# Optimization experiments

Measured on AMD Instinct MI355X. Metric: run time of the kernel, lower is better.

Reference implementation:

```python
import jax, jax.numpy as jnp
import numpy as np

NUM_EXPERTS = 8
TOP_K = 2
AUX_COEF = 0.01
B, S, D, H = 4, 2048, 1024, 684


def setup_inputs() -> dict:
    key = jax.random.key(0)
    ks = jax.random.split(key, 5)
    scale_d = 1.0 / np.sqrt(D)
    scale_h = 1.0 / np.sqrt(H)
    return {
        "x": jax.random.normal(ks[0], (B, S, D), dtype=jnp.float32),
        "router_w": jax.random.normal(ks[1], (NUM_EXPERTS, D), dtype=jnp.float32) * scale_d,
        "w1": jax.random.normal(ks[2], (NUM_EXPERTS, H, D), dtype=jnp.float32) * scale_d,
        "w2": jax.random.normal(ks[3], (NUM_EXPERTS, D, H), dtype=jnp.float32) * scale_h,
        "w3": jax.random.normal(ks[4], (NUM_EXPERTS, H, D), dtype=jnp.float32) * scale_d,
    }


def reference(x, router_w, w1, w2, w3):
    b, s, d = x.shape
    xf = x.reshape(-1, d)                                   # [T, d]
    probs = jax.nn.softmax(xf @ router_w.T, axis=-1)        # [T, E]
    topk_probs, topk_idx = jax.lax.top_k(probs, TOP_K)      # [T, k]

    # aux load-balancing loss (uses top-1 assignment density)
    density = jnp.mean(jax.nn.one_hot(topk_idx[:, 0], NUM_EXPERTS, dtype=xf.dtype), axis=0)
    aux_loss = AUX_COEF * jnp.sum(density * probs.mean(axis=0)) * NUM_EXPERTS

    # per-token per-expert combine weight (sums probs if an expert repeats across slots)
    combine = jnp.sum(jax.nn.one_hot(topk_idx, NUM_EXPERTS, dtype=xf.dtype)
                      * topk_probs[..., None], axis=1)      # [T, E]

    out = jnp.zeros_like(xf)
    for e in range(NUM_EXPERTS):  # fixed small expert loop
        h = jax.nn.silu(xf @ w1[e].T) * (xf @ w3[e].T)      # [T, H] SwiGLU
        out = out + combine[:, e:e + 1] * (h @ w2[e].T)     # weighted scatter-combine
    return out.reshape(b, s, d), aux_loss
```

## Files before the change

### kernel.cpp

```cpp
#include <hip/hip_runtime.h>
#include <hip/hip_bf16.h>

#define T_TOK 8192
#define DMODEL 1024
#define HDIM 684
#define HPAD 704
#define NEXP 8

typedef short  bf16x8  __attribute__((ext_vector_type(8)));
typedef float  f32x4   __attribute__((ext_vector_type(4)));

__device__ inline unsigned short f2bu(float f) {
    __hip_bfloat16 h = __float2bfloat16(f);
    return *reinterpret_cast<unsigned short*>(&h);
}

typedef const __attribute__((address_space(1))) unsigned int* gas_p;
typedef __attribute__((address_space(3))) unsigned int* las_p;
__device__ inline void ld_lds16(const unsigned short* g, unsigned short* l) {
    __builtin_amdgcn_global_load_lds((gas_p)g, (las_p)l, 16, 0, 0);
}

#define POS_OFF    74252800ull
#define PAIRS_OFF  74318336ull
#define WS_NEED   141427200ull

__global__ __launch_bounds__(256) void cvt_all(
    const float* __restrict__ w1, const float* __restrict__ w3, const float* __restrict__ w2,
    unsigned short* __restrict__ w1b, unsigned short* __restrict__ w3b,
    unsigned short* __restrict__ w2b, int n4, int n2)
{
    int i = blockIdx.x * 256 + threadIdx.x;
    if (i < 2 * n4) {
        const float* src; unsigned short* dst; int j;
        if (i < n4) { src = w1; dst = w1b; j = i; }
        else        { src = w3; dst = w3b; j = i - n4; }
        float4 v = ((const float4*)src)[j];
        ((ushort4*)dst)[j] = make_ushort4(f2bu(v.x), f2bu(v.y), f2bu(v.z), f2bu(v.w));
        return;
    }
    int j = i - 2 * n4;
    if (j >= n2) return;
    int row = j / 176;
    int col = (j - row * 176) * 4;
    ushort4 o = make_ushort4(0, 0, 0, 0);
    if (col < HDIM) {
        float4 v = *(const float4*)(w2 + (size_t)row * HDIM + col);
        o = make_ushort4(f2bu(v.x), f2bu(v.y), f2bu(v.z), f2bu(v.w));
    }
    *(ushort4*)(w2b + (size_t)row * HPAD + col) = o;
}

__global__ __launch_bounds__(256) void moe_router(
    const float* __restrict__ x, const float* __restrict__ rw,
    unsigned short* __restrict__ xb,
    float* __restrict__ blk_psum, int* __restrict__ blk_t1, int* __restrict__ blk_pc,
    int* __restrict__ topk_idx, float* __restrict__ topk_p)
{
    __shared__ float sp[4][NEXP];
    __shared__ int   si1[4], si2[4];

    int lane = threadIdx.x & 63;
    int w    = threadIdx.x >> 6;
    int t    = blockIdx.x * 4 + w;
    const float4* xr4 = (const float4*)(x + (size_t)t * DMODEL);
    ushort4* xbr4 = (ushort4*)(xb + (size_t)t * DMODEL);

    float acc[NEXP];
#pragma unroll
    for (int e = 0; e < NEXP; ++e) acc[e] = 0.f;
#pragma unroll
    for (int j = 0; j < DMODEL / 256; ++j) {
        float4 xv = xr4[j * 64 + lane];
        xbr4[j * 64 + lane] = make_ushort4(f2bu(xv.x), f2bu(xv.y), f2bu(xv.z), f2bu(xv.w));
#pragma unroll
        for (int e = 0; e < NEXP; ++e) {
            float4 rv = ((const float4*)(rw + (size_t)e * DMODEL))[j * 64 + lane];
            acc[e] += xv.x * rv.x + xv.y * rv.y + xv.z * rv.z + xv.w * rv.w;
        }
    }
#pragma unroll
    for (int off = 32; off > 0; off >>= 1) {
#pragma unroll
        for (int e = 0; e < NEXP; ++e)
            acc[e] += __shfl_xor(acc[e], off, 64);
    }
    if (lane == 0) {
        float m = acc[0];
#pragma unroll
        for (int e = 1; e < NEXP; ++e) m = fmaxf(m, acc[e]);
        float p[NEXP]; float s = 0.f;
#pragma unroll
        for (int e = 0; e < NEXP; ++e) { p[e] = expf(acc[e] - m); s += p[e]; }
        float inv = 1.f / s;
#pragma unroll
        for (int e = 0; e < NEXP; ++e) p[e] *= inv;
        int i1 = 0;
#pragma unroll
        for (int e = 1; e < NEXP; ++e) if (p[e] > p[i1]) i1 = e;
        int i2 = (i1 == 0) ? 1 : 0;
#pragma unroll
        for (int e = 0; e < NEXP; ++e) if (e != i1 && p[e] > p[i2]) i2 = e;

        topk_idx[t * 2 + 0] = i1;  topk_idx[t * 2 + 1] = i2;
        topk_p[t * 2 + 0] = p[i1]; topk_p[t * 2 + 1] = p[i2];
#pragma unroll
        for (int e = 0; e < NEXP; ++e) sp[w][e] = p[e];
        si1[w] = i1; si2[w] = i2;
    }
    __syncthreads();
    if (threadIdx.x < NEXP) {
        int e = threadIdx.x;
        float ps = sp[0][e] + sp[1][e] + sp[2][e] + sp[3][e];
        int t1 = (si1[0] == e) + (si1[1] == e) + (si1[2] == e) + (si1[3] == e);
        int pc = t1 + (si2[0] == e) + (si2[1] == e) + (si2[2] == e) + (si2[3] == e);
        blk_psum[blockIdx.x * NEXP + e] = ps;
        blk_t1[blockIdx.x * NEXP + e]  = t1;
        blk_pc[blockIdx.x * NEXP + e]  = pc;
    }
}

__global__ __launch_bounds__(256) void moe_scan(
    const float* __restrict__ blk_psum, const int* __restrict__ blk_t1,
    const int* __restrict__ blk_pc,
    int* pair_count, int* offsets, int* cursor, float* aux_out)
{
    __shared__ float wp[4][NEXP];
    __shared__ int   wt[4][NEXP], wc[4][NEXP];
    __shared__ float tp[NEXP];
    __shared__ int   tt1[NEXP], tpc[NEXP];

    int tid = threadIdx.x;
    int lane = tid & 63, w = tid >> 6;
    float lp[NEXP]; int lt[NEXP], lc[NEXP];
#pragma unroll
    for (int e = 0; e < NEXP; ++e) { lp[e] = 0.f; lt[e] = 0; lc[e] = 0; }
    for (int b = tid; b < 2048; b += 256)
#pragma unroll
        for (int e = 0; e < NEXP; ++e) {
            lp[e] += blk_psum[b * NEXP + e];
            lt[e] += blk_t1[b * NEXP + e];
            lc[e] += blk_pc[b * NEXP + e];
        }
#pragma unroll
    for (int off = 32; off > 0; off >>= 1) {
#pragma unroll
        for (int e = 0; e < NEXP; ++e) {
            lp[e] += __shfl_xor(lp[e], off, 64);
            lt[e] += __shfl_xor(lt[e], off, 64);
            lc[e] += __shfl_xor(lc[e], off, 64);
        }
    }
    if (lane == 0) {
#pragma unroll
        for (int e = 0; e < NEXP; ++e) { wp[w][e] = lp[e]; wt[w][e] = lt[e]; wc[w][e] = lc[e]; }
    }
    __syncthreads();
    if (tid < NEXP) {
        int e = tid;
        float s = wp[0][e] + wp[1][e] + wp[2][e] + wp[3][e];
        int t1 = wt[0][e] + wt[1][e] + wt[2][e] + wt[3][e];
        int pc = wc[0][e] + wc[1][e] + wc[2][e] + wc[3][e];
        tp[e] = s; tt1[e] = t1; tpc[e] = pc;
        pair_count[e] = pc;
    }
    __syncthreads();
    if (tid == 0) {
        int run = 0;
        for (int e = 0; e < NEXP; ++e) { offsets[e] = run; cursor[e] = run; run += tpc[e]; }
        float s = 0.f;
        for (int e = 0; e < NEXP; ++e)
            s += ((float)tt1[e] / (float)T_TOK) * (tp[e] / (float)T_TOK);
        aux_out[0] = 0.01f * s * (float)NEXP;
    }
}

__global__ __launch_bounds__(256) void moe_scatter(
    const int* __restrict__ topk_idx, const float* __restrict__ topk_p,
    int* cursor, int* __restrict__ pair_token, float* __restrict__ pair_prob,
    int* __restrict__ pos)
{
    __shared__ int lcnt[NEXP], gbase[NEXP];
    int tid = threadIdx.x;
    if (tid < NEXP) lcnt[tid] = 0;
    __syncthreads();
    int t = blockIdx.x * 256 + tid;
    int e0 = topk_idx[t * 2 + 0], e1 = topk_idx[t * 2 + 1];
    int p0 = atomicAdd(&lcnt[e0], 1);
    int p1 = atomicAdd(&lcnt[e1], 1);
    __syncthreads();
    if (tid < NEXP) gbase[tid] = atomicAdd(&cursor[tid], lcnt[tid]);
    __syncthreads();
    int q0 = gbase[e0] + p0, q1 = gbase[e1] + p1;
    pair_token[q0] = t; pair_prob[q0] = topk_p[t * 2 + 0];
    pair_token[q1] = t; pair_prob[q1] = topk_p[t * 2 + 1];
    pos[t * 2 + 0] = q0; pos[t * 2 + 1] = q1;
}


__global__ __launch_bounds__(512, 2) void moe_ffn1(
    const unsigned short* __restrict__ xb, const unsigned short* __restrict__ w1b,
    const unsigned short* __restrict__ w3b,
    const int* __restrict__ pair_count, const int* __restrict__ offsets,
    const int* __restrict__ pair_token,
    unsigned short* __restrict__ h)
{
    int e   = blockIdx.z;
    int cnt = pair_count[e];
    int m0  = blockIdx.y * 128;
    if (m0 >= cnt) return;
    int base = offsets[e];
    int n0   = blockIdx.x * 256;

    __shared__ unsigned short aT [3 * 4096];
    __shared__ unsigned short b1T[3 * 8192];
    __shared__ unsigned short b3T[3 * 8192];

    int tid  = threadIdx.x;
    int lane = tid & 63, wave = tid >> 6;
    int wm = wave >> 2, wn = wave & 3;

    int srow = lane >> 2;
    int ksg  = (lane & 3) ^ ((lane >> 3) & 3);
    int ar = m0 + wave * 16 + srow; if (ar >= cnt) ar = cnt - 1;
    const unsigned short* ap = xb + (size_t)pair_token[base + ar] * DMODEL + ksg * 8;
    int br0 = n0 + wave * 32 + srow;      if (br0 > HDIM - 1) br0 = HDIM - 1;
    int br1 = n0 + wave * 32 + srow + 16; if (br1 > HDIM - 1) br1 = HDIM - 1;
    const unsigned short* b1p0 = w1b + ((size_t)e * HDIM + br0) * DMODEL + ksg * 8;
    const unsigned short* b1p1 = w1b + ((size_t)e * HDIM + br1) * DMODEL + ksg * 8;
    const unsigned short* b3p0 = w3b + ((size_t)e * HDIM + br0) * DMODEL + ksg * 8;
    const unsigned short* b3p1 = w3b + ((size_t)e * HDIM + br1) * DMODEL + ksg * 8;

#define STAGE_F1(slot, koff) do { \
    ld_lds16(ap   + (koff), aT  + (slot) * 4096 + wave * 512); \
    ld_lds16(b1p0 + (koff), b1T + (slot) * 8192 + wave * 1024); \
    ld_lds16(b1p1 + (koff), b1T + (slot) * 8192 + wave * 1024 + 512); \
    ld_lds16(b3p0 + (koff), b3T + (slot) * 8192 + wave * 1024); \
    ld_lds16(b3p1 + (koff), b3T + (slot) * 8192 + wave * 1024 + 512); \
  } while (0)

    f32x4 acc1[4][4], acc3[4][4];
#pragma unroll
    for (int i = 0; i < 4; ++i)
#pragma unroll
        for (int j = 0; j < 4; ++j) { acc1[i][j] = (f32x4)(0.f); acc3[i][j] = (f32x4)(0.f); }

    int fr  = lane & 15;
    int sz8 = ((lane >> 4) ^ ((fr >> 1) & 3)) * 8;

    STAGE_F1(0, 0);
    STAGE_F1(1, 32);

    const int NIT = DMODEL / 32;
    for (int it = 0; it < NIT; ++it) {
        int slot = it % 3;
        if (it + 1 < NIT) asm volatile("s_waitcnt vmcnt(5)" ::: "memory");
        else              asm volatile("s_waitcnt vmcnt(0)" ::: "memory");
        __builtin_amdgcn_s_barrier();
        asm volatile("" ::: "memory");

        const unsigned short* cA  = aT  + slot * 4096;
        const unsigned short* cB1 = b1T + slot * 8192;
        const unsigned short* cB3 = b3T + slot * 8192;

        bf16x8 aF[4];
#pragma unroll
        for (int i = 0; i < 4; ++i)
            aF[i] = *(const bf16x8*)&cA[(wm * 64 + i * 16 + fr) * 32 + sz8];
        __builtin_amdgcn_s_setprio(1);
#pragma unroll
        for (int j = 0; j < 4; ++j) {
            int row = (wn * 64 + j * 16 + fr) * 32 + sz8;
            bf16x8 b1F = *(const bf16x8*)&cB1[row];
            bf16x8 b3F = *(const bf16x8*)&cB3[row];
#pragma unroll
            for (int i = 0; i < 4; ++i) {
                acc1[i][j] = __builtin_amdgcn_mfma_f32_16x16x32_bf16(aF[i], b1F, acc1[i][j], 0, 0, 0);
                acc3[i][j] = __builtin_amdgcn_mfma_f32_16x16x32_bf16(aF[i], b3F, acc3[i][j], 0, 0, 0);
            }
        }
        __builtin_amdgcn_s_setprio(0);

        if (it + 2 < NIT) STAGE_F1((it + 2) % 3, (it + 2) * 32);
    }
#undef STAGE_F1

    int cbase = n0 + wn * 64 + fr;
    int rbase = m0 + wm * 64 + (lane >> 4) * 4;
#pragma unroll
    for (int i = 0; i < 4; ++i) {
#pragma unroll
        for (int r = 0; r < 4; ++r) {
            int gr = rbase + i * 16 + r;
            if (gr >= cnt) continue;
            unsigned short* hrow = h + (size_t)(base + gr) * HPAD;
#pragma unroll
            for (int j = 0; j < 4; ++j) {
                int col = cbase + j * 16;
                if (col >= HPAD) continue;
                float v1 = acc1[i][j][r];
                float hv = (col < HDIM) ? (v1 / (1.f + expf(-v1))) * acc3[i][j][r] : 0.f;
                hrow[col] = f2bu(hv);
            }
        }
    }
}

__global__ __launch_bounds__(512, 2) void moe_ffn2(
    const unsigned short* __restrict__ h, const unsigned short* __restrict__ w2b,
    const int* __restrict__ pair_count, const int* __restrict__ offsets,
    const int* __restrict__ pair_token, const float* __restrict__ pair_prob,
    float* __restrict__ pairs_out, float* __restrict__ out, int use_atomic)
{
    int e   = blockIdx.z;
    int cnt = pair_count[e];
    int m0  = blockIdx.y * 256;
    if (m0 >= cnt) return;
    int base = offsets[e];
    int n0   = blockIdx.x * 256;

    __shared__ unsigned short aT[4 * 8192];
    __shared__ unsigned short bT[4 * 8192];

    int tid  = threadIdx.x;
    int lane = tid & 63, wave = tid >> 6;
    int wm = wave >> 2, wn = wave & 3;

    int srow = lane >> 2;
    int ksg  = (lane & 3) ^ ((lane >> 3) & 3);
    int ar0 = m0 + wave * 32 + srow;      if (ar0 >= cnt) ar0 = cnt - 1;
    int ar1 = m0 + wave * 32 + srow + 16; if (ar1 >= cnt) ar1 = cnt - 1;
    const unsigned short* ap0 = h + (size_t)(base + ar0) * HPAD + ksg * 8;
    const unsigned short* ap1 = h + (size_t)(base + ar1) * HPAD + ksg * 8;
    int brr = n0 + wave * 32 + srow;
    const unsigned short* bp0 = w2b + ((size_t)e * DMODEL + brr)      * HPAD + ksg * 8;
    const unsigned short* bp1 = w2b + ((size_t)e * DMODEL + brr + 16) * HPAD + ksg * 8;

#define STAGE_F2(slot, koff) do { \
    ld_lds16(ap0 + (koff), aT + (slot) * 8192 + wave * 1024); \
    ld_lds16(ap1 + (koff), aT + (slot) * 8192 + wave * 1024 + 512); \
    ld_lds16(bp0 + (koff), bT + (slot) * 8192 + wave * 1024); \
    ld_lds16(bp1 + (koff), bT + (slot) * 8192 + wave * 1024 + 512); \
  } while (0)

    f32x4 acc[8][4];
#pragma unroll
    for (int i = 0; i < 8; ++i)
#pragma unroll
        for (int j = 0; j < 4; ++j) acc[i][j] = (f32x4)(0.f);

    int fr  = lane & 15;
    int sz8 = ((lane >> 4) ^ ((fr >> 1) & 3)) * 8;

    STAGE_F2(0, 0);
    STAGE_F2(1, 32);
    STAGE_F2(2, 64);

    const int NIT = HPAD / 32;
    for (int it = 0; it < NIT; ++it) {
        int slot = it % 4;
        if      (it < NIT - 2) asm volatile("s_waitcnt vmcnt(8)" ::: "memory");
        else if (it == NIT - 2) asm volatile("s_waitcnt vmcnt(4)" ::: "memory");
        else                    asm volatile("s_waitcnt vmcnt(0)" ::: "memory");
        __builtin_amdgcn_s_barrier();
        asm volatile("" ::: "memory");

        const unsigned short* cA = aT + slot * 8192;
        const unsigned short* cB = bT + slot * 8192;

        bf16x8 aF[8];
#pragma unroll
        for (int i = 0; i < 8; ++i)
            aF[i] = *(const bf16x8*)&cA[(wm * 128 + i * 16 + fr) * 32 + sz8];
        __builtin_amdgcn_s_setprio(1);
#pragma unroll
        for (int j = 0; j < 4; ++j) {
            bf16x8 bF = *(const bf16x8*)&cB[(wn * 64 + j * 16 + fr) * 32 + sz8];
#pragma unroll
            for (int i = 0; i < 8; ++i)
                acc[i][j] = __builtin_amdgcn_mfma_f32_16x16x32_bf16(aF[i], bF, acc[i][j], 0, 0, 0);
        }
        __builtin_amdgcn_s_setprio(0);

        if (it + 3 < NIT) STAGE_F2((it + 3) % 4, (it + 3) * 32);
    }
#undef STAGE_F2

    int cbase = n0 + wn * 64 + fr;
    int rbase = m0 + wm * 128 + (lane >> 4) * 4;
#pragma unroll
    for (int i = 0; i < 8; ++i) {
#pragma unroll
        for (int r = 0; r < 4; ++r) {
            int gr = rbase + i * 16 + r;
            if (gr >= cnt) continue;
            int gp = base + gr;
            float pw = pair_prob[gp];
            if (!use_atomic) {
                float* prow = pairs_out + (size_t)gp * DMODEL;
#pragma unroll
                for (int j = 0; j < 4; ++j)
                    prow[cbase + j * 16] = pw * acc[i][j][r];
            } else {
                float* orow = out + (size_t)pair_token[gp] * DMODEL;
#pragma unroll
                for (int j = 0; j < 4; ++j)
                    atomicAdd(&orow[cbase + j * 16], pw * acc[i][j][r]);
            }
        }
    }
}

__global__ __launch_bounds__(256) void moe_combine(
    const float* __restrict__ pairs_out, const int* __restrict__ pos,
    float* __restrict__ out)
{
    int t = blockIdx.x;
    int c = threadIdx.x;
    int q0 = pos[t * 2 + 0], q1 = pos[t * 2 + 1];
    float4 a = ((const float4*)(pairs_out + (size_t)q0 * DMODEL))[c];
    float4 b = ((const float4*)(pairs_out + (size_t)q1 * DMODEL))[c];
    float4 o;
    o.x = a.x + b.x; o.y = a.y + b.y; o.z = a.z + b.z; o.w = a.w + b.w;
    ((float4*)(out + (size_t)t * DMODEL))[c] = o;
}

extern "C" void kernel_launch(void* const* d_in, const int* in_sizes, int n_in,
                              void* d_out, int out_size, void* d_ws, size_t ws_size,
                              hipStream_t stream)
{
    const float* x  = (const float*)d_in[0];
    const float* rw = (const float*)d_in[1];
    const float* w1 = (const float*)d_in[2];
    const float* w2 = (const float*)d_in[3];
    const float* w3 = (const float*)d_in[4];
    float* out = (float*)d_out;

    char* ws = (char*)d_ws;
    int*   pair_count = (int*)(ws + 0);
    int*   offsets    = (int*)(ws + 32);
    int*   cursor     = (int*)(ws + 64);
    float* blk_psum   = (float*)(ws + 256);
    int*   blk_t1     = (int*)(ws + 65792);
    int*   blk_pc     = (int*)(ws + 131328);
    int*   topk_idx   = (int*)(ws + 196864);
    float* topk_p     = (float*)(ws + 262400);
    int*   pair_token = (int*)(ws + 327936);
    float* pair_prob  = (float*)(ws + 393472);
    unsigned short* xb  = (unsigned short*)(ws + 459264);
    unsigned short* w1b = (unsigned short*)(ws + 17236480);
    unsigned short* w3b = (unsigned short*)(ws + 28443136);
    unsigned short* w2b = (unsigned short*)(ws + 39649792);
    unsigned short* hbuf= (unsigned short*)(ws + 51184128);
    int*   pos        = (int*)(ws + POS_OFF);
    float* pairs_out  = (float*)(ws + PAIRS_OFF);

    int two_pass = (ws_size >= WS_NEED) ? 1 : 0;
    if (!two_pass)
        hipMemsetAsync(d_out, 0, (size_t)out_size * sizeof(float), stream);

    int n4 = NEXP * HDIM * DMODEL / 4;
    int n2 = NEXP * DMODEL * (HPAD / 4);
    cvt_all<<<(2 * n4 + n2 + 255) / 256, 256, 0, stream>>>(w1, w3, w2, w1b, w3b, w2b, n4, n2);

    moe_router <<<T_TOK / 4, 256, 0, stream>>>(x, rw, xb, blk_psum, blk_t1, blk_pc, topk_idx, topk_p);
    moe_scan   <<<1, 256, 0, stream>>>(blk_psum, blk_t1, blk_pc, pair_count, offsets, cursor,
                                       out + (size_t)T_TOK * DMODEL);
    moe_scatter<<<T_TOK / 256, 256, 0, stream>>>(topk_idx, topk_p, cursor, pair_token, pair_prob, pos);

    moe_ffn1<<<dim3(3, 128, 8), 512, 0, stream>>>(xb, w1b, w3b, pair_count, offsets, pair_token, hbuf);
    moe_ffn2<<<dim3(4, 64, 8), 512, 0, stream>>>(hbuf, w2b, pair_count, offsets, pair_token, pair_prob,
                                                 pairs_out, out, two_pass ? 0 : 1);
    if (two_pass)
        moe_combine<<<T_TOK, 256, 0, stream>>>(pairs_out, pos, out);
}
```

Measured before the change: 319.7 us.

## Shrink MoE FFN GEMM tiles and restructure into 4-slot two-barrier pipeline

Both expert GEMM kernels now use 128x128 (ffn1) and 128x256 (ffn2) output tiles instead of 128x256 and 256x256. Each thread stages one 16-byte chunk per operand per slot through a 4-deep LDS ring. All fragments are read from LDS before the next stage is issued, and barriers fence both sides of the MFMA block. The aim is more blocks, lower LDS and register pressure, and deeper prefetch that hides global-load latency. The cost is less data reuse per tile and an extra barrier every k-step.

```diff
diff --git a/kernel.cpp b/kernel.cpp
--- a/kernel.cpp
+++ b/kernel.cpp
@@ -210,96 +210,98 @@
     int m0  = blockIdx.y * 128;
     if (m0 >= cnt) return;
     int base = offsets[e];
-    int n0   = blockIdx.x * 256;
-
-    __shared__ unsigned short aT [3 * 4096];
-    __shared__ unsigned short b1T[3 * 8192];
-    __shared__ unsigned short b3T[3 * 8192];
+    int n0   = blockIdx.x * 128;
+
+    __shared__ unsigned short aT [4 * 4096];
+    __shared__ unsigned short b1T[4 * 4096];
+    __shared__ unsigned short b3T[4 * 4096];
 
     int tid  = threadIdx.x;
     int lane = tid & 63, wave = tid >> 6;
     int wm = wave >> 2, wn = wave & 3;
 
-    int srow = lane >> 2;
-    int ksg  = (lane & 3) ^ ((lane >> 3) & 3);
-    int ar = m0 + wave * 16 + srow; if (ar >= cnt) ar = cnt - 1;
+    int r   = tid >> 2;
+    int ksg = (tid & 3) ^ ((tid >> 3) & 3);
+    int ar = m0 + r; if (ar >= cnt) ar = cnt - 1;
     const unsigned short* ap = xb + (size_t)pair_token[base + ar] * DMODEL + ksg * 8;
-    int br0 = n0 + wave * 32 + srow;      if (br0 > HDIM - 1) br0 = HDIM - 1;
-    int br1 = n0 + wave * 32 + srow + 16; if (br1 > HDIM - 1) br1 = HDIM - 1;
-    const unsigned short* b1p0 = w1b + ((size_t)e * HDIM + br0) * DMODEL + ksg * 8;
-    const unsigned short* b1p1 = w1b + ((size_t)e * HDIM + br1) * DMODEL + ksg * 8;
-    const unsigned short* b3p0 = w3b + ((size_t)e * HDIM + br0) * DMODEL + ksg * 8;
-    const unsigned short* b3p1 = w3b + ((size_t)e * HDIM + br1) * DMODEL + ksg * 8;
-
-#define STAGE_F1(slot, koff) do { \
-    ld_lds16(ap   + (koff), aT  + (slot) * 4096 + wave * 512); \
-    ld_lds16(b1p0 + (koff), b1T + (slot) * 8192 + wave * 1024); \
-    ld_lds16(b1p1 + (koff), b1T + (slot) * 8192 + wave * 1024 + 512); \
-    ld_lds16(b3p0 + (koff), b3T + (slot) * 8192 + wave * 1024); \
-    ld_lds16(b3p1 + (koff), b3T + (slot) * 8192 + wave * 1024 + 512); \
-  } while (0)
-
-    f32x4 acc1[4][4], acc3[4][4];
+    int br = n0 + r; if (br > HDIM - 1) br = HDIM - 1;
+    const unsigned short* b1p = w1b + ((size_t)e * HDIM + br) * DMODEL + ksg * 8;
+    const unsigned short* b3p = w3b + ((size_t)e * HDIM + br) * DMODEL + ksg * 8;
+    unsigned short* da  = aT  + tid * 8;
+    unsigned short* db1 = b1T + tid * 8;
+    unsigned short* db3 = b3T + tid * 8;
+
+#define STG1(slot, kof) do { \
+    ld_lds16(ap  + (kof), da  + (slot) * 4096); \
+    ld_lds16(b1p + (kof), db1 + (slot) * 4096); \
+    ld_lds16(b3p + (kof), db3 + (slot) * 4096); } while (0)
+
+    f32x4 acc1[4][2], acc3[4][2];
 #pragma unroll
     for (int i = 0; i < 4; ++i)
 #pragma unroll
-        for (int j = 0; j < 4; ++j) { acc1[i][j] = (f32x4)(0.f); acc3[i][j] = (f32x4)(0.f); }
+        for (int j = 0; j < 2; ++j) { acc1[i][j] = (f32x4)(0.f); acc3[i][j] = (f32x4)(0.f); }
 
     int fr  = lane & 15;
     int sz8 = ((lane >> 4) ^ ((fr >> 1) & 3)) * 8;
 
-    STAGE_F1(0, 0);
-    STAGE_F1(1, 32);
-
-    const int NIT = DMODEL / 32;
-    for (int it = 0; it < NIT; ++it) {
-        int slot = it % 3;
-        if (it + 1 < NIT) asm volatile("s_waitcnt vmcnt(5)" ::: "memory");
-        else              asm volatile("s_waitcnt vmcnt(0)" ::: "memory");
+    STG1(0, 0); STG1(1, 32); STG1(2, 64);
+    asm volatile("s_waitcnt vmcnt(6)" ::: "memory");
+    __builtin_amdgcn_s_barrier();
+    asm volatile("" ::: "memory");
+
+    const int P = DMODEL / 32;
+    for (int p = 0; p < P; ++p) {
+        int slot = p & 3;
+        if (p + 2 < P) asm volatile("s_waitcnt vmcnt(3)" ::: "memory");
+        else           asm volatile("s_waitcnt vmcnt(0)" ::: "memory");
+
+        const unsigned short* cA  = aT  + slot * 4096;
+        const unsigned short* cB1 = b1T + slot * 4096;
+        const unsigned short* cB3 = b3T + slot * 4096;
+
+        bf16x8 aF[4], b1F[2], b3F[2];
+#pragma unroll
+        for (int i = 0; i < 4; ++i)
+            aF[i] = *(const bf16x8*)&cA[(wm * 64 + i * 16 + fr) * 32 + sz8];
+#pragma unroll
+        for (int j = 0; j < 2; ++j) {
+            b1F[j] = *(const bf16x8*)&cB1[(wn * 32 + j * 16 + fr) * 32 + sz8];
+            b3F[j] = *(const bf16x8*)&cB3[(wn * 32 + j * 16 + fr) * 32 + sz8];
+        }
+        if (p + 3 < P) STG1((p + 3) & 3, (p + 3) * 32);
+
         __builtin_amdgcn_s_barrier();
         asm volatile("" ::: "memory");
-
-        const unsigned short* cA  = aT  + slot * 4096;
-        const unsigned short* cB1 = b1T + slot * 8192;
-        const unsigned short* cB3 = b3T + slot * 8192;
-
-        bf16x8 aF[4];
-#pragma unroll
-        for (int i = 0; i < 4; ++i)
-            aF[i] = *(const bf16x8*)&cA[(wm * 64 + i * 16 + fr) * 32 + sz8];
         __builtin_amdgcn_s_setprio(1);
 #pragma unroll
-        for (int j = 0; j < 4; ++j) {
-            int row = (wn * 64 + j * 16 + fr) * 32 + sz8;
-            bf16x8 b1F = *(const bf16x8*)&cB1[row];
-            bf16x8 b3F = *(const bf16x8*)&cB3[row];
+        for (int j = 0; j < 2; ++j)
 #pragma unroll
             for (int i = 0; i < 4; ++i) {
-                acc1[i][j] = __builtin_amdgcn_mfma_f32_16x16x32_bf16(aF[i], b1F, acc1[i][j], 0, 0, 0);
-                acc3[i][j] = __builtin_amdgcn_mfma_f32_16x16x32_bf16(aF[i], b3F, acc3[i][j], 0, 0, 0);
+                acc1[i][j] = __builtin_amdgcn_mfma_f32_16x16x32_bf16(aF[i], b1F[j], acc1[i][j], 0, 0, 0);
+                acc3[i][j] = __builtin_amdgcn_mfma_f32_16x16x32_bf16(aF[i], b3F[j], acc3[i][j], 0, 0, 0);
             }
-        }
         __builtin_amdgcn_s_setprio(0);
-
-        if (it + 2 < NIT) STAGE_F1((it + 2) % 3, (it + 2) * 32);
-    }
-#undef STAGE_F1
-
-    int cbase = n0 + wn * 64 + fr;
+        __builtin_amdgcn_s_barrier();
+        asm volatile("" ::: "memory");
+    }
+#undef STG1
+
+    int cbase = n0 + wn * 32 + fr;
     int rbase = m0 + wm * 64 + (lane >> 4) * 4;
 #pragma unroll
     for (int i = 0; i < 4; ++i) {
 #pragma unroll
-        for (int r = 0; r < 4; ++r) {
-            int gr = rbase + i * 16 + r;
+        for (int rr = 0; rr < 4; ++rr) {
+            int gr = rbase + i * 16 + rr;
             if (gr >= cnt) continue;
             unsigned short* hrow = h + (size_t)(base + gr) * HPAD;
 #pragma unroll
-            for (int j = 0; j < 4; ++j) {
+            for (int j = 0; j < 2; ++j) {
                 int col = cbase + j * 16;
                 if (col >= HPAD) continue;
-                float v1 = acc1[i][j][r];
-                float hv = (col < HDIM) ? (v1 / (1.f + expf(-v1))) * acc3[i][j][r] : 0.f;
+                float v1 = acc1[i][j][rr];
+                float hv = (col < HDIM) ? (v1 / (1.f + expf(-v1))) * acc3[i][j][rr] : 0.f;
                 hrow[col] = f2bu(hv);
             }
         }
@@ -314,85 +316,85 @@
 {
     int e   = blockIdx.z;
     int cnt = pair_count[e];
-    int m0  = blockIdx.y * 256;
+    int m0  = blockIdx.y * 128;
     if (m0 >= cnt) return;
     int base = offsets[e];
     int n0   = blockIdx.x * 256;
 
-    __shared__ unsigned short aT[4 * 8192];
+    __shared__ unsigned short aT[4 * 4096];
     __shared__ unsigned short bT[4 * 8192];
 
     int tid  = threadIdx.x;
     int lane = tid & 63, wave = tid >> 6;
     int wm = wave >> 2, wn = wave & 3;
 
-    int srow = lane >> 2;
-    int ksg  = (lane & 3) ^ ((lane >> 3) & 3);
-    int ar0 = m0 + wave * 32 + srow;      if (ar0 >= cnt) ar0 = cnt - 1;
-    int ar1 = m0 + wave * 32 + srow + 16; if (ar1 >= cnt) ar1 = cnt - 1;
-    const unsigned short* ap0 = h + (size_t)(base + ar0) * HPAD + ksg * 8;
-    const unsigned short* ap1 = h + (size_t)(base + ar1) * HPAD + ksg * 8;
-    int brr = n0 + wave * 32 + srow;
-    const unsigned short* bp0 = w2b + ((size_t)e * DMODEL + brr)      * HPAD + ksg * 8;
-    const unsigned short* bp1 = w2b + ((size_t)e * DMODEL + brr + 16) * HPAD + ksg * 8;
-
-#define STAGE_F2(slot, koff) do { \
-    ld_lds16(ap0 + (koff), aT + (slot) * 8192 + wave * 1024); \
-    ld_lds16(ap1 + (koff), aT + (slot) * 8192 + wave * 1024 + 512); \
-    ld_lds16(bp0 + (koff), bT + (slot) * 8192 + wave * 1024); \
-    ld_lds16(bp1 + (koff), bT + (slot) * 8192 + wave * 1024 + 512); \
-  } while (0)
-
-    f32x4 acc[8][4];
-#pragma unroll
-    for (int i = 0; i < 8; ++i)
+    int r   = tid >> 2;
+    int ksg = (tid & 3) ^ ((tid >> 3) & 3);
+    int ar = m0 + r; if (ar >= cnt) ar = cnt - 1;
+    const unsigned short* ap  = h + (size_t)(base + ar) * HPAD + ksg * 8;
+    const unsigned short* bp0 = w2b + ((size_t)e * DMODEL + n0 + r)       * HPAD + ksg * 8;
+    const unsigned short* bp1 = w2b + ((size_t)e * DMODEL + n0 + r + 128) * HPAD + ksg * 8;
+    unsigned short* da = aT + tid * 8;
+    unsigned short* db = bT + tid * 8;
+
+#define STG2(slot, kof) do { \
+    ld_lds16(ap  + (kof), da + (slot) * 4096); \
+    ld_lds16(bp0 + (kof), db + (slot) * 8192); \
+    ld_lds16(bp1 + (kof), db + (slot) * 8192 + 4096); } while (0)
+
+    f32x4 acc[4][4];
+#pragma unroll
+    for (int i = 0; i < 4; ++i)
 #pragma unroll
         for (int j = 0; j < 4; ++j) acc[i][j] = (f32x4)(0.f);
 
     int fr  = lane & 15;
     int sz8 = ((lane >> 4) ^ ((fr >> 1) & 3)) * 8;
 
-    STAGE_F2(0, 0);
-    STAGE_F2(1, 32);
-    STAGE_F2(2, 64);
-
-    const int NIT = HPAD / 32;
-    for (int it = 0; it < NIT; ++it) {
-        int slot = it % 4;
-        if      (it < NIT - 2) asm volatile("s_waitcnt vmcnt(8)" ::: "memory");
-        else if (it == NIT - 2) asm volatile("s_waitcnt vmcnt(4)" ::: "memory");
-        else                    asm volatile("s_waitcnt vmcnt(0)" ::: "memory");
+    STG2(0, 0); STG2(1, 32); STG2(2, 64);
+    asm volatile("s_waitcnt vmcnt(6)" ::: "memory");
+    __builtin_amdgcn_s_barrier();
+    asm volatile("" ::: "memory");
+
+    const int P = HPAD / 32;
+    for (int p = 0; p < P; ++p) {
+        int slot = p & 3;
+        if (p + 2 < P) asm volatile("s_waitcnt vmcnt(3)" ::: "memory");
+        else           asm volatile("s_waitcnt vmcnt(0)" ::: "memory");
+
+        const unsigned short* cA = aT + slot * 4096;
+        const unsigned short* cB = bT + slot * 8192;
+
+        bf16x8 aF[4], bF[4];
+#pragma unroll
+        for (int i = 0; i < 4; ++i)
+            aF[i] = *(const bf16x8*)&cA[(wm * 64 + i * 16 + fr) * 32 + sz8];
+#pragma unroll
+        for (int j = 0; j < 4; ++j)
+            bF[j] = *(const bf16x8*)&cB[(wn * 64 + j * 16 + fr) * 32 + sz8];
+        if (p + 3 < P) STG2((p + 3) & 3, (p + 3) * 32);
+
         __builtin_amdgcn_s_barrier();
         asm volatile("" ::: "memory");
-
-        const unsigned short* cA = aT + slot * 8192;
-        const unsigned short* cB = bT + slot * 8192;
-
-        bf16x8 aF[8];
-#pragma unroll
-        for (int i = 0; i < 8; ++i)
-            aF[i] = *(const bf16x8*)&cA[(wm * 128 + i * 16 + fr) * 32 + sz8];
         __builtin_amdgcn_s_setprio(1);
 #pragma unroll
-        for (int j = 0; j < 4; ++j) {
-            bf16x8 bF = *(const bf16x8*)&cB[(wn * 64 + j * 16 + fr) * 32 + sz8];
-#pragma unroll
-            for (int i = 0; i < 8; ++i)
-                acc[i][j] = __builtin_amdgcn_mfma_f32_16x16x32_bf16(aF[i], bF, acc[i][j], 0, 0, 0);
-        }
+        for (int j = 0; j < 4; ++j)
+#pragma unroll
+            for (int i = 0; i < 4; ++i)
+                acc[i][j] = __builtin_amdgcn_mfma_f32_16x16x32_bf16(aF[i], bF[j], acc[i][j], 0, 0, 0);
         __builtin_amdgcn_s_setprio(0);
-
-        if (it + 3 < NIT) STAGE_F2((it + 3) % 4, (it + 3) * 32);
-    }
-#undef STAGE_F2
+        __builtin_amdgcn_s_barrier();
+        asm volatile("" ::: "memory");
+    }
+#undef STG2
 
     int cbase = n0 + wn * 64 + fr;
-    int rbase = m0 + wm * 128 + (lane >> 4) * 4;
-#pragma unroll
-    for (int i = 0; i < 8; ++i) {
-#pragma unroll
-        for (int r = 0; r < 4; ++r) {
-            int gr = rbase + i * 16 + r;
+    int rbase = m0 + wm * 64 + (lane >> 4) * 4;
+#pragma unroll
+    for (int i = 0; i < 4; ++i) {
+#pragma unroll
+        for (int rr = 0; rr < 4; ++rr) {
+            int gr = rbase + i * 16 + rr;
             if (gr >= cnt) continue;
             int gp = base + gr;
             float pw = pair_prob[gp];
@@ -400,12 +402,12 @@
                 float* prow = pairs_out + (size_t)gp * DMODEL;
 #pragma unroll
                 for (int j = 0; j < 4; ++j)
-                    prow[cbase + j * 16] = pw * acc[i][j][r];
+                    prow[cbase + j * 16] = pw * acc[i][j][rr];
             } else {
                 float* orow = out + (size_t)pair_token[gp] * DMODEL;
 #pragma unroll
                 for (int j = 0; j < 4; ++j)
-                    atomicAdd(&orow[cbase + j * 16], pw * acc[i][j][r]);
+                    atomicAdd(&orow[cbase + j * 16], pw * acc[i][j][rr]);
             }
         }
     }
@@ -468,7 +470,7 @@
                                        out + (size_t)T_TOK * DMODEL);
     moe_scatter<<<T_TOK / 256, 256, 0, stream>>>(topk_idx, topk_p, cursor, pair_token, pair_prob, pos);
 
-    moe_ffn1<<<dim3(3, 128, 8), 512, 0, stream>>>(xb, w1b, w3b, pair_count, offsets, pair_token, hbuf);
+    moe_ffn1<<<dim3(6, 64, 8), 512, 0, stream>>>(xb, w1b, w3b, pair_count, offsets, pair_token, hbuf);
     moe_ffn2<<<dim3(4, 64, 8), 512, 0, stream>>>(hbuf, w2b, pair_count, offsets, pair_token, pair_prob,
                                                  pairs_out, out, two_pass ? 0 : 1);
     if (two_pass)
```

Result: slower. 336.8 us (+5.4%).
